# Kernel tuning notes

Hardware: AMD Instinct MI355X
Metric: run time of the kernel (lower is better)

## Reference

```python
import jax, jax.numpy as jnp
import numpy as np

N = 100000   # nodes
E = 1600000  # edges per relation
D = 128      # feature dim (dim_in == dim_out)
H = 128      # semantic-attention hidden size
R = 3        # relations


def setup_inputs() -> dict:
    key = jax.random.key(0)
    ks = jax.random.split(key, 16)
    inp = {"x": jax.random.normal(ks[0], (N, D), jnp.float32)}
    for r in range(R):
        inp[f"src{r}"] = jax.random.randint(ks[1 + 2 * r], (E,), 0, N)
        inp[f"dst{r}"] = jax.random.randint(ks[2 + 2 * r], (E,), 0, N)
        inp[f"W{r}"] = jax.random.normal(ks[7 + r], (D, D), jnp.float32) / np.sqrt(D)
    inp["aW"] = jax.random.normal(ks[10], (D, H), jnp.float32) / np.sqrt(D)
    inp["ab"] = jnp.zeros((H,), jnp.float32)
    inp["aq"] = jax.random.normal(ks[11], (H,), jnp.float32) / np.sqrt(H)
    return inp


def _gcn_rel(x, W, src, dst):
    # DGL GraphConv with norm='both', no bias:
    # out = D_in^{-1/2} . A . D_out^{-1/2} . X . W   (degrees clamped to >= 1)
    ones = jnp.ones(src.shape, dtype=x.dtype)
    deg_out = jnp.maximum(jax.ops.segment_sum(ones, src, num_segments=N), 1.0)
    deg_in = jnp.maximum(jax.ops.segment_sum(ones, dst, num_segments=N), 1.0)
    h = (x @ W) * jax.lax.rsqrt(deg_out)[:, None]          # (N, D)
    agg = jax.ops.segment_sum(h[src], dst, num_segments=N)  # gather->scatter (E, D)
    return agg * jax.lax.rsqrt(deg_in)[:, None]


def reference(x, W0, W1, W2, aW, ab, aq, src0, dst0, src1, dst1, src2, dst2):
    # per-relation message passing, stacked over relation axis: (N, R, D)
    z = jnp.stack([
        _gcn_rel(x, W0, src0, dst0),
        _gcn_rel(x, W1, src1, dst1),
        _gcn_rel(x, W2, src2, dst2),
    ], axis=1)
    # SemanticAttention: w_r = mean_n( tanh(z W1 + b) @ q );  beta = softmax(w)
    proj = jnp.tanh(jnp.einsum('nrd,dh->nrh', z, aW) + ab)   # (N, R, H)
    w = jnp.einsum('nrh,h->r', proj, aq) / z.shape[0]        # (R,)
    beta = jax.nn.softmax(w)
    return jnp.einsum('nrd,r->nd', z, beta)                  # (N, D)
```

## Files before the change

### kernel.cpp

```cpp
#include <hip/hip_runtime.h>
#include <hip/hip_bf16.h>

#define NN 100000
#define EE 1600000
#define DD 128
#define RNG 8
#define RSZ 12500
#define CAPR 16
#define CHK 32

typedef __attribute__((ext_vector_type(8))) short bf16x8;
typedef __attribute__((ext_vector_type(4))) float f32x4;
union FB { unsigned u[4]; uint4 u4; bf16x8 v; };

__device__ inline unsigned f2bf(float x){unsigned u=__float_as_uint(x);return (u+0x7fffu+((u>>16)&1u))>>16;}
__device__ inline unsigned bf16pack(float a,float b){return (f2bf(b)<<16)|(f2bf(a)&0xffffu);}
__device__ inline unsigned packsplit(float v){unsigned hb=f2bf(v);float hf=__uint_as_float(hb<<16);unsigned lb=f2bf(v-hf);return (hb<<16)|(lb&0xffffu);}
__device__ inline float bflo(unsigned u){return __uint_as_float(u<<16);}
__device__ inline float bfhi(unsigned u){return __uint_as_float(u&0xffff0000u);}

struct Bufs {
  const float* x;
  const int *s0,*d0,*s1,*d1,*s2,*d2;
  const float *W0,*W1,*W2,*aW,*ab,*aq;
  unsigned *h0,*h1,*h2;
  unsigned *zb0,*zb1;
  ushort *csr0,*csr1;
  int *cursor;
  float *wpart;
  float *rs;
  int *histpart;
  ushort *fhi,*flo;
  float *out;
};

__global__ __launch_bounds__(256) void k0_kernel(Bufs B) {
  __shared__ unsigned bins[RSZ/2];
  int b = blockIdx.x;
  if (b < 768) {
    int range = b & 7, chunk = (b >> 3) & 31, rel = b >> 8;
    const int* src = rel==0?B.s0: rel==1?B.s1:B.s2;
    for (int i=threadIdx.x;i<RSZ/2;i+=256) bins[i]=0;
    __syncthreads();
    int lo = range*RSZ, e0 = chunk*(EE/CHK);
    for (int e=e0+(int)threadIdx.x; e<e0+EE/CHK; e+=256){
      int v = src[e]-lo;
      if ((unsigned)v<(unsigned)RSZ) atomicAdd(&bins[v>>1], 1u<<((v&1)*16));
    }
    __syncthreads();
    int* outp = B.histpart + ((size_t)(rel*CHK+chunk))*NN + lo;
    for (int i=threadIdx.x;i<RSZ;i+=256) outp[i] = (bins[i>>1]>>((i&1)*16)) & 0xffff;
  } else if (b < 768+587) {
    int id = b-768;
    const int Z = 3*NN*RNG + 4;
    int* dst = B.cursor;
#pragma unroll
    for (int k=0;k<4;++k){
      int off = id*4096 + k*1024 + (int)threadIdx.x*4;
      if (off+4 <= Z) *(int4*)(dst+off) = make_int4(0,0,0,0);
      else { for (int j=0;j<4;++j) if (off+j<Z) dst[off+j]=0; }
    }
  } else {
    int m = b - (768+587);
    const float* W = m==0?B.W0: m==1?B.W1: m==2?B.W2: B.aW;
    ushort* ho = B.fhi + (size_t)m*16384;
    ushort* lp = B.flo + (size_t)m*16384;
    for (int idx=threadIdx.x; idx<16384; idx+=256){
      int j=idx&7, lane=(idx>>3)&63, ft=(idx>>9)&7, ks=idx>>12;
      int k = ks*32 + (lane>>4)*8 + j;
      int f = ft*16 + (lane&15);
      float v = W[k*128+f];
      unsigned hb = f2bf(v);
      float hf = __uint_as_float(hb<<16);
      ho[idx]=(ushort)hb; lp[idx]=(ushort)f2bf(v-hf);
    }
  }
}

__device__ inline void do_bucket(int id, int rel, const Bufs& B) {
  const int* src = rel==0?B.s0: rel==1?B.s1:B.s2;
  const int* dst = rel==0?B.d0: rel==1?B.d1:B.d2;
  int* cur = B.cursor + (size_t)rel*NN*RNG;
  ushort* csr = (rel==1)? B.csr1 : B.csr0;
  int e0 = id*512;
  for (int e=e0+(int)threadIdx.x; e<e0+512; e+=256){
    int s = src[e], d = dst[e];
    int rg = s / RSZ;
    int pos = atomicAdd(&cur[d*RNG+rg], 1);
    if (pos < CAPR) csr[((size_t)d*RNG+rg)*CAPR + pos] = (ushort)(s - rg*RSZ);
  }
}

__device__ inline void do_reduce(int id, const Bufs& B) {
  int tid = id*256 + threadIdx.x;
  if (tid >= 3*NN) return;
  int rel = tid/NN, n = tid-rel*NN;
  const int* p = B.histpart + (size_t)rel*CHK*NN + n;
  int s = 0;
#pragma unroll
  for (int c=0;c<CHK;++c) s += p[(size_t)c*NN];
  B.rs[tid] = rsqrtf(fmaxf((float)s, 1.f));
}

__device__ inline void do_gemm0(int tile, int rel, const Bufs& B, unsigned (*As)[132]) {
  const uint4* Bhi = (const uint4*)(B.fhi + (size_t)rel*16384);
  const uint4* Blo = (const uint4*)(B.flo + (size_t)rel*16384);
  unsigned* h = rel==0?B.h0: rel==1?B.h1:B.h2;
  int t = threadIdx.x, row0 = tile*32;
  for (int idx=t; idx<32*32; idx+=256){
    int r = idx>>5, c4 = (idx&31)<<2;
    float4 v = *(const float4*)(B.x + (size_t)(row0+r)*DD + c4);
    uint4 pk; pk.x=packsplit(v.x); pk.y=packsplit(v.y); pk.z=packsplit(v.z); pk.w=packsplit(v.w);
    *(uint4*)&As[r][c4] = pk;
  }
  __syncthreads();
  int wv=t>>6, l=t&63, ln=l&15, lk=l>>4;
  int nrow=(wv&1)*16+ln, fh=wv>>1;
  f32x4 acc[4];
#pragma unroll
  for (int i=0;i<4;++i) acc[i] = (f32x4){0.f,0.f,0.f,0.f};
#pragma unroll
  for (int ks=0;ks<4;++ks){
    unsigned u[8];
    int kd = ks*32 + lk*8;
    *(uint4*)&u[0] = *(const uint4*)&As[nrow][kd];
    *(uint4*)&u[4] = *(const uint4*)&As[nrow][kd+4];
    FB bh, bl;
#pragma unroll
    for (int i=0;i<4;++i){
      bh.u[i] = (u[2*i]>>16) | (u[2*i+1]&0xffff0000u);
      bl.u[i] = (u[2*i]&0xffffu) | (u[2*i+1]<<16);
    }
#pragma unroll
    for (int fi=0;fi<4;++fi){
      int ft = fh*4+fi;
      FB wh, wl;
      wh.u4 = Bhi[(ks*8+ft)*64 + l];
      wl.u4 = Blo[(ks*8+ft)*64 + l];
      acc[fi] = __builtin_amdgcn_mfma_f32_16x16x32_bf16(wh.v, bh.v, acc[fi],0,0,0);
      acc[fi] = __builtin_amdgcn_mfma_f32_16x16x32_bf16(wl.v, bh.v, acc[fi],0,0,0);
      acc[fi] = __builtin_amdgcn_mfma_f32_16x16x32_bf16(wh.v, bl.v, acc[fi],0,0,0);
    }
  }
  int node = row0+nrow;
#pragma unroll
  for (int fi=0;fi<4;++fi){
    int ft = fh*4+fi;
    uint2 o;
    o.x = bf16pack(acc[fi][0], acc[fi][1]);
    o.y = bf16pack(acc[fi][2], acc[fi][3]);
    *(uint2*)(h + (size_t)node*64 + ft*8 + lk*2) = o;
  }
}

__device__ inline void do_gather(int id, int rel, const Bufs& B) {
  int node = id*4 + (threadIdx.x>>6);
  int lane = threadIdx.x & 63;
  const int* cur = B.cursor + (size_t)rel*NN*RNG + (size_t)node*RNG;
  const ushort* csr = (rel==1)? B.csr1 : B.csr0;
  const unsigned* h = rel==0?B.h0: rel==1?B.h1:B.h2;
  int cnt[RNG];
  int deg = 0, maxc = 0;
#pragma unroll
  for (int k=0;k<RNG;++k){
    int c = cur[k];
    deg += c;
    c = min(c, CAPR);
    cnt[k] = c;
    maxc = max(maxc, c);
  }
  const ushort* base = csr + (size_t)node*(RNG*CAPR);
  float ax = 0.f, ay = 0.f;
  for (int s=0;s<maxc;++s){
    unsigned u[RNG];
#pragma unroll
    for (int k=0;k<RNG;++k){
      if (s < cnt[k]){
        int idx = k*RSZ + (int)base[k*CAPR + s];
        u[k] = h[(size_t)idx*64 + lane];
      }
    }
#pragma unroll
    for (int k=0;k<RNG;++k){
      if (s < cnt[k]){ ax += bflo(u[k]); ay += bfhi(u[k]); }
    }
  }
  float sc = rsqrtf(fmaxf((float)deg, 1.f));
  if (rel < 2) {
    unsigned* zb = rel ? B.zb1 : B.zb0;
    zb[(size_t)node*64+lane] = bf16pack(ax*sc, ay*sc);
  } else {
    *(float2*)(B.out + (size_t)node*DD + lane*2) = make_float2(ax*sc, ay*sc);
  }
}

__device__ inline void do_g1b(int tile, int rel, const Bufs& B,
                              unsigned (*As)[68], float* red) {
  const unsigned* zb = rel ? B.zb1 : B.zb0;
  const uint4* Bhi = (const uint4*)(B.fhi + (size_t)3*16384);
  const uint4* Blo = (const uint4*)(B.flo + (size_t)3*16384);
  int t = threadIdx.x, row0 = tile*32;
  for (int idx=t; idx<32*16; idx+=256){
    int r = idx>>4, c4 = (idx&15)<<2;
    *(uint4*)&As[r][c4] = *(const uint4*)(zb + (size_t)(row0+r)*64 + c4);
  }
  __syncthreads();
  int wv=t>>6, l=t&63, ln=l&15, lk=l>>4;
  int nrow=(wv&1)*16+ln, fh=wv>>1;
  f32x4 acc[4];
#pragma unroll
  for (int i=0;i<4;++i) acc[i] = (f32x4){0.f,0.f,0.f,0.f};
#pragma unroll
  for (int ks=0;ks<4;++ks){
    FB bb; bb.u4 = *(const uint4*)&As[nrow][ks*16 + lk*4];
#pragma unroll
    for (int fi=0;fi<4;++fi){
      int ft = fh*4+fi;
      FB wh, wl;
      wh.u4 = Bhi[(ks*8+ft)*64 + l];
      wl.u4 = Blo[(ks*8+ft)*64 + l];
      acc[fi] = __builtin_amdgcn_mfma_f32_16x16x32_bf16(wh.v, bb.v, acc[fi],0,0,0);
      acc[fi] = __builtin_amdgcn_mfma_f32_16x16x32_bf16(wl.v, bb.v, acc[fi],0,0,0);
    }
  }
  float s = 0.f;
#pragma unroll
  for (int fi=0;fi<4;++fi){
#pragma unroll
    for (int r=0;r<4;++r){
      int f = (fh*4+fi)*16 + lk*4 + r;
      float v = acc[fi][r] + B.ab[f];
      float e = __expf(2.f*v);
      s += (1.f - 2.f/(e+1.f)) * B.aq[f];
    }
  }
#pragma unroll
  for (int m=1;m<64;m<<=1) s += __shfl_xor(s, m);
  if (l==0) red[wv] = s;
  __syncthreads();
  if (t==0) atomicAdd(B.wpart + rel, red[0]+red[1]+red[2]+red[3]);
}

__device__ inline void do_g1f(int tile, const Bufs& B,
                              unsigned (*As)[132], float* red) {
  const uint4* Bhi = (const uint4*)(B.fhi + (size_t)3*16384);
  const uint4* Blo = (const uint4*)(B.flo + (size_t)3*16384);
  int t = threadIdx.x, row0 = tile*32;
  for (int idx=t; idx<32*32; idx+=256){
    int r = idx>>5, c4 = (idx&31)<<2;
    float4 v = *(const float4*)(B.out + (size_t)(row0+r)*DD + c4);
    uint4 pk; pk.x=packsplit(v.x); pk.y=packsplit(v.y); pk.z=packsplit(v.z); pk.w=packsplit(v.w);
    *(uint4*)&As[r][c4] = pk;
  }
  __syncthreads();
  int wv=t>>6, l=t&63, ln=l&15, lk=l>>4;
  int nrow=(wv&1)*16+ln, fh=wv>>1;
  f32x4 acc[4];
#pragma unroll
  for (int i=0;i<4;++i) acc[i] = (f32x4){0.f,0.f,0.f,0.f};
#pragma unroll
  for (int ks=0;ks<4;++ks){
    unsigned u[8];
    int kd = ks*32 + lk*8;
    *(uint4*)&u[0] = *(const uint4*)&As[nrow][kd];
    *(uint4*)&u[4] = *(const uint4*)&As[nrow][kd+4];
    FB bh, bl;
#pragma unroll
    for (int i=0;i<4;++i){
      bh.u[i] = (u[2*i]>>16) | (u[2*i+1]&0xffff0000u);
      bl.u[i] = (u[2*i]&0xffffu) | (u[2*i+1]<<16);
    }
#pragma unroll
    for (int fi=0;fi<4;++fi){
      int ft = fh*4+fi;
      FB wh, wl;
      wh.u4 = Bhi[(ks*8+ft)*64 + l];
      wl.u4 = Blo[(ks*8+ft)*64 + l];
      acc[fi] = __builtin_amdgcn_mfma_f32_16x16x32_bf16(wh.v, bh.v, acc[fi],0,0,0);
      acc[fi] = __builtin_amdgcn_mfma_f32_16x16x32_bf16(wl.v, bh.v, acc[fi],0,0,0);
      acc[fi] = __builtin_amdgcn_mfma_f32_16x16x32_bf16(wh.v, bl.v, acc[fi],0,0,0);
    }
  }
  float s = 0.f;
#pragma unroll
  for (int fi=0;fi<4;++fi){
#pragma unroll
    for (int r=0;r<4;++r){
      int f = (fh*4+fi)*16 + lk*4 + r;
      float v = acc[fi][r] + B.ab[f];
      float e = __expf(2.f*v);
      s += (1.f - 2.f/(e+1.f)) * B.aq[f];
    }
  }
#pragma unroll
  for (int m=1;m<64;m<<=1) s += __shfl_xor(s, m);
  if (l==0) red[wv] = s;
  __syncthreads();
  if (t==0) atomicAdd(B.wpart + 2, red[0]+red[1]+red[2]+red[3]);
}

__global__ __launch_bounds__(256) void hscale_kernel(Bufs B) {
  int idx = blockIdx.x*256 + threadIdx.x;
  int gn = idx >> 4;
  float f = B.rs[gn];
  uint4* h4 = (uint4*)B.h0;
  uint4 u = h4[idx];
  u.x = bf16pack(bflo(u.x)*f, bfhi(u.x)*f);
  u.y = bf16pack(bflo(u.y)*f, bfhi(u.y)*f);
  u.z = bf16pack(bflo(u.z)*f, bfhi(u.z)*f);
  u.w = bf16pack(bflo(u.w)*f, bfhi(u.w)*f);
  h4[idx] = u;
}


__global__ __launch_bounds__(256) void megaA(Bufs B) {
  __shared__ unsigned As[32][132];
  const int n0=3125, n1=9375, n2=1172;
  const int tot = n0+n1+n2;
  int b = blockIdx.x;
  long f = ((long)b*n0)/tot;
  if (((long)(b+1)*n0)/tot > f){ do_bucket((int)f, 0, B); return; }
  int b1 = b-(int)f; int tt = tot-n0;
  f = ((long)b1*n1)/tt;
  if (((long)(b1+1)*n1)/tt > f){ int g=(int)f; do_gemm0(g%3125, g/3125, B, As); return; }
  do_reduce(b1-(int)f, B);
}

__global__ __launch_bounds__(256) void megaGB(Bufs B, int grel, int brel) {
  const int n0=25000, n1=3125;
  const int tot = n0+n1;
  int b = blockIdx.x;
  long f = ((long)b*n0)/tot;
  if (((long)(b+1)*n0)/tot > f) do_gather((int)f, grel, B);
  else                          do_bucket(b-(int)f, brel, B);
}

__global__ __launch_bounds__(256) void megaG(Bufs B) {
  do_gather(blockIdx.x, 2, B);
}

__global__ __launch_bounds__(256) void megaC(Bufs B) {
  __shared__ unsigned As[32][132];
  __shared__ float red[4];
  int b = blockIdx.x;
  if (b < 3125)      do_g1b(b, 0, B, (unsigned(*)[68])&As[0][0], red);
  else if (b < 6250) do_g1b(b-3125, 1, B, (unsigned(*)[68])&As[0][0], red);
  else               do_g1f(b-6250, B, As, red);
}

__global__ __launch_bounds__(256) void combine_kernel(Bufs B) {
  int tid = blockIdx.x*256 + threadIdx.x;
  float w0 = B.wpart[0]*(1.f/NN), w1 = B.wpart[1]*(1.f/NN), w2 = B.wpart[2]*(1.f/NN);
  float m = fmaxf(w0, fmaxf(w1,w2));
  float e0 = expf(w0-m), e1 = expf(w1-m), e2 = expf(w2-m);
  float inv = 1.f/(e0+e1+e2);
  float b0 = e0*inv, b1 = e1*inv, b2 = e2*inv;
  unsigned u0 = B.zb0[tid], u1 = B.zb1[tid];
  float2 c = ((const float2*)B.out)[tid];
  float2 o;
  o.x = b0*bflo(u0) + b1*bflo(u1) + b2*c.x;
  o.y = b0*bfhi(u0) + b1*bfhi(u1) + b2*c.y;
  ((float2*)B.out)[tid] = o;
}

extern "C" void kernel_launch(void* const* d_in, const int* in_sizes, int n_in,
                              void* d_out, int out_size, void* d_ws, size_t ws_size,
                              hipStream_t stream) {
  Bufs B;
  B.x  = (const float*)d_in[0];
  B.s0 = (const int*)d_in[1]; B.d0 = (const int*)d_in[2]; B.W0 = (const float*)d_in[3];
  B.s1 = (const int*)d_in[4]; B.d1 = (const int*)d_in[5]; B.W1 = (const float*)d_in[6];
  B.s2 = (const int*)d_in[7]; B.d2 = (const int*)d_in[8]; B.W2 = (const float*)d_in[9];
  B.aW = (const float*)d_in[10]; B.ab = (const float*)d_in[11]; B.aq = (const float*)d_in[12];
  B.out = (float*)d_out;

  char* p = (char*)d_ws;
  auto alloc = [&](size_t bytes){ char* r = p; p += (bytes + 255) & ~(size_t)255; return r; };
  B.zb0 = (unsigned*)alloc((size_t)NN*64*4);
  B.zb1 = (unsigned*)alloc((size_t)NN*64*4);
  B.h0  = (unsigned*)alloc((size_t)NN*64*4);
  B.h1  = (unsigned*)alloc((size_t)NN*64*4);
  B.h2  = (unsigned*)alloc((size_t)NN*64*4);
  B.csr0 = (ushort*)alloc((size_t)NN*RNG*CAPR*2);
  B.csr1 = (ushort*)alloc((size_t)NN*RNG*CAPR*2);
  B.cursor = (int*)alloc(((size_t)3*NN*RNG + 4)*4);
  B.wpart  = (float*)(B.cursor + (size_t)3*NN*RNG);
  B.rs  = (float*)alloc((size_t)3*NN*4);
  B.fhi = (ushort*)alloc((size_t)4*16384*2);
  B.flo = (ushort*)alloc((size_t)4*16384*2);
  B.histpart = (int*)B.zb0;

  k0_kernel<<<1359, 256, 0, stream>>>(B);
  megaA<<<3125+9375+1172, 256, 0, stream>>>(B);
  hscale_kernel<<<3*NN*16/256, 256, 0, stream>>>(B);
  megaGB<<<25000+3125, 256, 0, stream>>>(B, 0, 1);
  megaGB<<<25000+3125, 256, 0, stream>>>(B, 1, 2);
  megaG<<<25000, 256, 0, stream>>>(B);
  megaC<<<3125+3125+3125, 256, 0, stream>>>(B);
  combine_kernel<<<(NN*64)/256, 256, 0, stream>>>(B);
}
```

Before: 857.3 us.

## Store relation-2 result as bf16 and overlap attention GEMMs with gathers

Relation 2 aggregation now goes to a bf16 buffer (aliased onto h0) instead of fp32 output. That drops the split-precision three-MFMA path and unifies all three attention GEMMs into one LDS-free variant that reads directly from global memory with per-wave atomics. The h-scaling pass is split: relation 0 is scaled up front, and the rest is folded into the first gather/bucket mega-kernel. The attention GEMMs for relations 0 and 1 now run alongside the relation-2 gather. This cuts launches and idle tails, at the cost of lower precision for relation 2 and more global atomics.

```diff
diff --git a/kernel.cpp b/kernel.cpp
--- a/kernel.cpp
+++ b/kernel.cpp
@@ -24,7 +24,7 @@
   const int *s0,*d0,*s1,*d1,*s2,*d2;
   const float *W0,*W1,*W2,*aW,*ab,*aq;
   unsigned *h0,*h1,*h2;
-  unsigned *zb0,*zb1;
+  unsigned *zb0,*zb1,*zb2;
   ushort *csr0,*csr1;
   int *cursor;
   float *wpart;
@@ -186,33 +186,23 @@
     }
   }
   float sc = rsqrtf(fmaxf((float)deg, 1.f));
-  if (rel < 2) {
-    unsigned* zb = rel ? B.zb1 : B.zb0;
-    zb[(size_t)node*64+lane] = bf16pack(ax*sc, ay*sc);
-  } else {
-    *(float2*)(B.out + (size_t)node*DD + lane*2) = make_float2(ax*sc, ay*sc);
-  }
-}
-
-__device__ inline void do_g1b(int tile, int rel, const Bufs& B,
-                              unsigned (*As)[68], float* red) {
-  const unsigned* zb = rel ? B.zb1 : B.zb0;
+  unsigned* zb = rel==0?B.zb0: rel==1?B.zb1:B.zb2;
+  zb[(size_t)node*64+lane] = bf16pack(ax*sc, ay*sc);
+}
+
+__device__ inline void do_g1nl(int tile, int rel, const Bufs& B) {
+  const unsigned* zb = rel==0?B.zb0: rel==1?B.zb1:B.zb2;
   const uint4* Bhi = (const uint4*)(B.fhi + (size_t)3*16384);
   const uint4* Blo = (const uint4*)(B.flo + (size_t)3*16384);
-  int t = threadIdx.x, row0 = tile*32;
-  for (int idx=t; idx<32*16; idx+=256){
-    int r = idx>>4, c4 = (idx&15)<<2;
-    *(uint4*)&As[r][c4] = *(const uint4*)(zb + (size_t)(row0+r)*64 + c4);
-  }
-  __syncthreads();
-  int wv=t>>6, l=t&63, ln=l&15, lk=l>>4;
-  int nrow=(wv&1)*16+ln, fh=wv>>1;
+  int t = threadIdx.x, wv = t>>6, l = t&63, ln = l&15, lk = l>>4;
+  int nrow = (wv&1)*16 + ln, fh = wv>>1;
+  int node = tile*32 + nrow;
   f32x4 acc[4];
 #pragma unroll
   for (int i=0;i<4;++i) acc[i] = (f32x4){0.f,0.f,0.f,0.f};
 #pragma unroll
   for (int ks=0;ks<4;++ks){
-    FB bb; bb.u4 = *(const uint4*)&As[nrow][ks*16 + lk*4];
+    FB bb; bb.u4 = *(const uint4*)(zb + (size_t)node*64 + ks*16 + lk*4);
 #pragma unroll
     for (int fi=0;fi<4;++fi){
       int ft = fh*4+fi;
@@ -236,87 +226,26 @@
   }
 #pragma unroll
   for (int m=1;m<64;m<<=1) s += __shfl_xor(s, m);
-  if (l==0) red[wv] = s;
-  __syncthreads();
-  if (t==0) atomicAdd(B.wpart + rel, red[0]+red[1]+red[2]+red[3]);
-}
-
-__device__ inline void do_g1f(int tile, const Bufs& B,
-                              unsigned (*As)[132], float* red) {
-  const uint4* Bhi = (const uint4*)(B.fhi + (size_t)3*16384);
-  const uint4* Blo = (const uint4*)(B.flo + (size_t)3*16384);
-  int t = threadIdx.x, row0 = tile*32;
-  for (int idx=t; idx<32*32; idx+=256){
-    int r = idx>>5, c4 = (idx&31)<<2;
-    float4 v = *(const float4*)(B.out + (size_t)(row0+r)*DD + c4);
-    uint4 pk; pk.x=packsplit(v.x); pk.y=packsplit(v.y); pk.z=packsplit(v.z); pk.w=packsplit(v.w);
-    *(uint4*)&As[r][c4] = pk;
-  }
-  __syncthreads();
-  int wv=t>>6, l=t&63, ln=l&15, lk=l>>4;
-  int nrow=(wv&1)*16+ln, fh=wv>>1;
-  f32x4 acc[4];
-#pragma unroll
-  for (int i=0;i<4;++i) acc[i] = (f32x4){0.f,0.f,0.f,0.f};
-#pragma unroll
-  for (int ks=0;ks<4;++ks){
-    unsigned u[8];
-    int kd = ks*32 + lk*8;
-    *(uint4*)&u[0] = *(const uint4*)&As[nrow][kd];
-    *(uint4*)&u[4] = *(const uint4*)&As[nrow][kd+4];
-    FB bh, bl;
-#pragma unroll
-    for (int i=0;i<4;++i){
-      bh.u[i] = (u[2*i]>>16) | (u[2*i+1]&0xffff0000u);
-      bl.u[i] = (u[2*i]&0xffffu) | (u[2*i+1]<<16);
-    }
-#pragma unroll
-    for (int fi=0;fi<4;++fi){
-      int ft = fh*4+fi;
-      FB wh, wl;
-      wh.u4 = Bhi[(ks*8+ft)*64 + l];
-      wl.u4 = Blo[(ks*8+ft)*64 + l];
-      acc[fi] = __builtin_amdgcn_mfma_f32_16x16x32_bf16(wh.v, bh.v, acc[fi],0,0,0);
-      acc[fi] = __builtin_amdgcn_mfma_f32_16x16x32_bf16(wl.v, bh.v, acc[fi],0,0,0);
-      acc[fi] = __builtin_amdgcn_mfma_f32_16x16x32_bf16(wh.v, bl.v, acc[fi],0,0,0);
-    }
-  }
-  float s = 0.f;
-#pragma unroll
-  for (int fi=0;fi<4;++fi){
-#pragma unroll
-    for (int r=0;r<4;++r){
-      int f = (fh*4+fi)*16 + lk*4 + r;
-      float v = acc[fi][r] + B.ab[f];
-      float e = __expf(2.f*v);
-      s += (1.f - 2.f/(e+1.f)) * B.aq[f];
-    }
-  }
-#pragma unroll
-  for (int m=1;m<64;m<<=1) s += __shfl_xor(s, m);
-  if (l==0) red[wv] = s;
-  __syncthreads();
-  if (t==0) atomicAdd(B.wpart + 2, red[0]+red[1]+red[2]+red[3]);
-}
-
-__global__ __launch_bounds__(256) void hscale_kernel(Bufs B) {
-  int idx = blockIdx.x*256 + threadIdx.x;
-  int gn = idx >> 4;
+  if (l==0) atomicAdd(B.wpart + rel, s);
+}
+
+__device__ inline void do_hscale(int aidx, const Bufs& B) {
+  int gn = aidx >> 4;
   float f = B.rs[gn];
   uint4* h4 = (uint4*)B.h0;
-  uint4 u = h4[idx];
+  uint4 u = h4[aidx];
   u.x = bf16pack(bflo(u.x)*f, bfhi(u.x)*f);
   u.y = bf16pack(bflo(u.y)*f, bfhi(u.y)*f);
   u.z = bf16pack(bflo(u.z)*f, bfhi(u.z)*f);
   u.w = bf16pack(bflo(u.w)*f, bfhi(u.w)*f);
-  h4[idx] = u;
+  h4[aidx] = u;
 }
 
 
 __global__ __launch_bounds__(256) void megaA(Bufs B) {
   __shared__ unsigned As[32][132];
-  const int n0=3125, n1=9375, n2=1172;
-  const int tot = n0+n1+n2;
+  const int n0=3125, n1=9375;
+  const int tot = n0+n1+1172;
   int b = blockIdx.x;
   long f = ((long)b*n0)/tot;
   if (((long)(b+1)*n0)/tot > f){ do_bucket((int)f, 0, B); return; }
@@ -326,26 +255,40 @@
   do_reduce(b1-(int)f, B);
 }
 
-__global__ __launch_bounds__(256) void megaGB(Bufs B, int grel, int brel) {
+__global__ __launch_bounds__(256) void hscaleA_kernel(Bufs B) {
+  do_hscale(blockIdx.x*256 + threadIdx.x, B);
+}
+
+__global__ __launch_bounds__(256) void megaGBH(Bufs B) {
+  const int n0=25000, n1=3125;
+  const int tot = n0+n1+12500;
+  int b = blockIdx.x;
+  long f = ((long)b*n0)/tot;
+  if (((long)(b+1)*n0)/tot > f){ do_gather((int)f, 0, B); return; }
+  int b1 = b-(int)f; int tt = tot-n0;
+  f = ((long)b1*n1)/tt;
+  if (((long)(b1+1)*n1)/tt > f){ do_bucket((int)f, 1, B); return; }
+  do_hscale(NN*16 + (b1-(int)f)*256 + (int)threadIdx.x, B);
+}
+
+__global__ __launch_bounds__(256) void megaGB(Bufs B) {
   const int n0=25000, n1=3125;
   const int tot = n0+n1;
   int b = blockIdx.x;
   long f = ((long)b*n0)/tot;
-  if (((long)(b+1)*n0)/tot > f) do_gather((int)f, grel, B);
-  else                          do_bucket(b-(int)f, brel, B);
-}
-
-__global__ __launch_bounds__(256) void megaG(Bufs B) {
-  do_gather(blockIdx.x, 2, B);
+  if (((long)(b+1)*n0)/tot > f) do_gather((int)f, 1, B);
+  else                          do_bucket(b-(int)f, 2, B);
+}
+
+__global__ __launch_bounds__(256) void megaGT(Bufs B) {
+  int b = blockIdx.x;
+  if (b < 25000)      do_gather(b, 2, B);
+  else if (b < 28125) do_g1nl(b-25000, 0, B);
+  else                do_g1nl(b-28125, 1, B);
 }
 
 __global__ __launch_bounds__(256) void megaC(Bufs B) {
-  __shared__ unsigned As[32][132];
-  __shared__ float red[4];
-  int b = blockIdx.x;
-  if (b < 3125)      do_g1b(b, 0, B, (unsigned(*)[68])&As[0][0], red);
-  else if (b < 6250) do_g1b(b-3125, 1, B, (unsigned(*)[68])&As[0][0], red);
-  else               do_g1f(b-6250, B, As, red);
+  do_g1nl(blockIdx.x, 2, B);
 }
 
 __global__ __launch_bounds__(256) void combine_kernel(Bufs B) {
@@ -355,11 +298,10 @@
   float e0 = expf(w0-m), e1 = expf(w1-m), e2 = expf(w2-m);
   float inv = 1.f/(e0+e1+e2);
   float b0 = e0*inv, b1 = e1*inv, b2 = e2*inv;
-  unsigned u0 = B.zb0[tid], u1 = B.zb1[tid];
-  float2 c = ((const float2*)B.out)[tid];
+  unsigned u0 = B.zb0[tid], u1 = B.zb1[tid], u2 = B.zb2[tid];
   float2 o;
-  o.x = b0*bflo(u0) + b1*bflo(u1) + b2*c.x;
-  o.y = b0*bfhi(u0) + b1*bfhi(u1) + b2*c.y;
+  o.x = b0*bflo(u0) + b1*bflo(u1) + b2*bflo(u2);
+  o.y = b0*bfhi(u0) + b1*bfhi(u1) + b2*bfhi(u2);
   ((float2*)B.out)[tid] = o;
 }
 
@@ -389,13 +331,14 @@
   B.fhi = (ushort*)alloc((size_t)4*16384*2);
   B.flo = (ushort*)alloc((size_t)4*16384*2);
   B.histpart = (int*)B.zb0;
+  B.zb2 = B.h0;
 
   k0_kernel<<<1359, 256, 0, stream>>>(B);
   megaA<<<3125+9375+1172, 256, 0, stream>>>(B);
-  hscale_kernel<<<3*NN*16/256, 256, 0, stream>>>(B);
-  megaGB<<<25000+3125, 256, 0, stream>>>(B, 0, 1);
-  megaGB<<<25000+3125, 256, 0, stream>>>(B, 1, 2);
-  megaG<<<25000, 256, 0, stream>>>(B);
-  megaC<<<3125+3125+3125, 256, 0, stream>>>(B);
+  hscaleA_kernel<<<NN*16/256, 256, 0, stream>>>(B);
+  megaGBH<<<25000+3125+12500, 256, 0, stream>>>(B);
+  megaGB<<<25000+3125, 256, 0, stream>>>(B);
+  megaGT<<<25000+3125+3125, 256, 0, stream>>>(B);
+  megaC<<<3125, 256, 0, stream>>>(B);
   combine_kernel<<<(NN*64)/256, 256, 0, stream>>>(B);
 }
```

Result: slower. 1.278 ms (+49.1%).
